# Kernel tuning notes

Hardware: AMD Instinct MI355X
Metric: run time of the kernel (lower is better)

The kernel has to match this reference:

```python
import jax, jax.numpy as jnp
import numpy as np
from functools import partial

# Static configuration (must match setup_inputs / init_kwargs)
N_CLOUDS = 16      # number of point clouds in the batch
PTS = 16384        # points per cloud (uniform, batch vector is repeat(arange(B), PTS))
RATIO = 0.25       # EncodeLayer ratio
M = int(PTS * RATIO)  # samples per cloud = 4096


def _fps_one(p, m):
    """Farthest point sampling on one cloud p:[n,3] -> local indices [m].
    Matches torch_geometric fps with random_start=False semantics: start at point 0,
    then iteratively pick the point with max min-distance to the selected set."""
    d0 = jnp.sum((p - p[0]) ** 2, axis=-1)  # squared dist to first pick, [n]

    def step(dists, _):
        idx = jnp.argmax(dists)
        new_d = jnp.sum((p - p[idx]) ** 2, axis=-1)
        return jnp.minimum(dists, new_d), idx

    _, idxs = jax.lax.scan(step, d0, None, length=m - 1)
    return jnp.concatenate([jnp.zeros((1,), dtype=idxs.dtype), idxs])


def setup_inputs() -> dict:
    key = jax.random.key(0)
    k1, k2 = jax.random.split(key)
    pos = jax.random.normal(k1, (N_CLOUDS * PTS, 3), dtype=jnp.float32)
    feats = jax.random.normal(k2, (N_CLOUDS * PTS, 128), dtype=jnp.float32)
    batch = jnp.repeat(jnp.arange(N_CLOUDS, dtype=jnp.int64), PTS)
    return {"pos": pos, "feats": feats, "batch": batch}


def reference(pos, feats, batch):
    # pos:[N,3]; batch assumed uniform with N_CLOUDS clouds of PTS points each.
    pos_b = pos.reshape(N_CLOUDS, PTS, 3)
    local = jax.vmap(partial(_fps_one, m=M))(pos_b)  # [B, M] local indices
    offsets = (jnp.arange(N_CLOUDS, dtype=local.dtype) * PTS)[:, None]
    samples = (local + offsets).reshape(-1)  # global flat indices, like torch_geometric fps
    return samples
```

## Files before the change

### kernel.cpp

```cpp
#include <hip/hip_runtime.h>

#define N_CLOUDS 16
#define PTS      16384
#define M        4096
#define FPS_THREADS  1024
#define NWAVES   (FPS_THREADS / 64)
#define PPT      16
#define SORT_THREADS 512

typedef float v2f __attribute__((ext_vector_type(2)));
typedef unsigned long long u64;
typedef unsigned int u32;
typedef unsigned short u16;


#define PAIRS8_X(X) X(0) X(1) X(2) X(3) X(4) X(5) X(6) X(7)

#define DPP_MAX_STEP(key, CTRL) { \
        const u32 lo_  = (u32)(key); \
        const u32 hi_  = (u32)((key) >> 32); \
        const u32 lo2_ = (u32)__builtin_amdgcn_update_dpp(0, (int)lo_, (CTRL), 0xf, 0xf, false); \
        const u32 hi2_ = (u32)__builtin_amdgcn_update_dpp(0, (int)hi_, (CTRL), 0xf, 0xf, false); \
        const u64 ok_  = ((u64)hi2_ << 32) | lo2_; \
        (key) = (ok_ > (key)) ? ok_ : (key); \
    }

#define DPP_FMIN_STEP(v, CTRL) { \
        const int t_ = __builtin_amdgcn_update_dpp(__float_as_int(v), __float_as_int(v), (CTRL), 0xf, 0xf, false); \
        (v) = fminf((v), __int_as_float(t_)); \
    }
#define DPP_FMAX_STEP(v, CTRL) { \
        const int t_ = __builtin_amdgcn_update_dpp(__float_as_int(v), __float_as_int(v), (CTRL), 0xf, 0xf, false); \
        (v) = fmaxf((v), __int_as_float(t_)); \
    }
#define DPP_RED6(MACRO, v) \
        MACRO(v, 0x111) MACRO(v, 0x112) MACRO(v, 0x114) MACRO(v, 0x118) \
        MACRO(v, 0x142) MACRO(v, 0x143)

__global__ __launch_bounds__(SORT_THREADS)
void sort_kernel(const float* __restrict__ pos, float* __restrict__ pos_s,
                 u16* __restrict__ mapT)
{
    __shared__ u32 keys[PTS];
    const int cloud = blockIdx.x;
    const int tid   = threadIdx.x;
    const int ln    = tid & 63;
    const size_t b3 = (size_t)cloud * PTS * 3;

    float mn = 1e30f, mx = -1e30f;
    for (int s = 0; s < PTS / SORT_THREADS; ++s) {
        const float x = pos[b3 + (size_t)(tid + s * SORT_THREADS) * 3];
        mn = fminf(mn, x);
        mx = fmaxf(mx, x);
    }
    DPP_RED6(DPP_FMIN_STEP, mn)
    DPP_RED6(DPP_FMAX_STEP, mx)
    float* red = (float*)keys;
    const int nw = SORT_THREADS / 64;
    if (ln == 63) { red[tid >> 6] = mn; red[nw + (tid >> 6)] = mx; }
    __syncthreads();
    float xmin = red[0], xmax = red[nw];
    for (int w = 1; w < nw; ++w) {
        xmin = fminf(xmin, red[w]);
        xmax = fmaxf(xmax, red[nw + w]);
    }
    __syncthreads();

    const float scale = 262143.0f / fmaxf(xmax - xmin, 1e-30f);
    for (int s = 0; s < PTS / SORT_THREADS; ++s) {
        const int i = tid + s * SORT_THREADS;
        const float x = pos[b3 + (size_t)i * 3];
        const u32 q = (u32)fminf(fmaxf((x - xmin) * scale, 0.0f), 262143.0f);
        keys[i] = (q << 14) | (u32)i;
    }

    for (u32 k = 2; k <= (u32)PTS; k <<= 1) {
        for (u32 j = k >> 1; j; j >>= 1) {
            __syncthreads();
            for (int s = 0; s < PTS / SORT_THREADS; ++s) {
                const u32 i = (u32)(tid + s * SORT_THREADS);
                const u32 p = i ^ j;
                if (p > i) {
                    const u32 a = keys[i], b = keys[p];
                    if (((i & k) == 0) == (a > b)) { keys[i] = b; keys[p] = a; }
                }
            }
        }
    }
    __syncthreads();

    for (int c = 0; c < 2; ++c) {
        u32 loc[PPT];
        const int cb = tid * 32 + c * PPT;
        for (int s = 0; s < PPT; ++s) loc[s] = keys[cb + s] & (u32)(PTS - 1);
        for (int a = 1; a < PPT; ++a) {
            const u32 v = loc[a];
            int b = a;
            while (b > 0 && loc[b - 1] > v) { loc[b] = loc[b - 1]; --b; }
            loc[b] = v;
        }
        for (int s = 0; s < PPT; ++s) keys[cb + s] = loc[s];
    }
    __syncthreads();

    for (int s = 0; s < PTS / SORT_THREADS; ++s) {
        const int i = tid + s * SORT_THREADS;
        const u32 orig = keys[i];
        mapT[(size_t)cloud * PTS + (size_t)(i & (PPT - 1)) * FPS_THREADS + (i >> 4)] = (u16)orig;
        const size_t so = b3 + (size_t)i * 3;
        const size_t oo = b3 + (size_t)orig * 3;
        pos_s[so + 0] = pos[oo + 0];
        pos_s[so + 1] = pos[oo + 1];
        pos_s[so + 2] = pos[oo + 2];
    }
}

template<bool SORTED>
__global__ __launch_bounds__(FPS_THREADS)
__attribute__((amdgpu_waves_per_eu(4, 4)))
void fps_kernel(const float* __restrict__ pos,
                const float* __restrict__ psrc,
                const u16* __restrict__ mapT,
                int* __restrict__ out)
{
#pragma clang fp contract(off)
    const int cloud = blockIdx.x;
    const int tid   = threadIdx.x;
    const int base  = cloud * PTS;
    const int wave  = tid >> 6;
    const int lane  = tid & 63;

    __shared__ u64 skey[2][NWAVES];
    __shared__ __attribute__((aligned(16))) u16 mlds[PTS];

    if constexpr (SORTED) {
        const uint4* src = (const uint4*)(mapT + (size_t)cloud * PTS);
        uint4* dst = (uint4*)mlds;
#pragma unroll
        for (int s = 0; s < PTS * 2 / 16 / FPS_THREADS; ++s)
            dst[s * FPS_THREADS + tid] = src[s * FPS_THREADS + tid];
        __syncthreads();
    }

    const float q0x = pos[(size_t)base * 3 + 0];
    const float q0y = pos[(size_t)base * 3 + 1];
    const float q0z = pos[(size_t)base * 3 + 2];
    v2f qx2 = {q0x, q0x}, qy2 = {q0y, q0y}, qz2 = {q0z, q0z};

    const float4* pos4 = (const float4*)psrc;
    const int fo = cloud * (PTS * 3 / 4) + tid * (PPT * 3 / 4);

#define DECL(j) v2f XX##j, YY##j, ZZ##j, DD##j;
    PAIRS8_X(DECL)
#undef DECL

#define QUADLOAD(q, j0, j1) { \
        const float4 fa = pos4[fo + 3*(q) + 0]; \
        const float4 fb = pos4[fo + 3*(q) + 1]; \
        const float4 fc = pos4[fo + 3*(q) + 2]; \
        XX##j0 = (v2f){fa.x, fa.w}; \
        YY##j0 = (v2f){fa.y, fb.x}; \
        ZZ##j0 = (v2f){fa.z, fb.y}; \
        XX##j1 = (v2f){fb.z, fc.y}; \
        YY##j1 = (v2f){fb.w, fc.z}; \
        ZZ##j1 = (v2f){fc.x, fc.w}; }
    QUADLOAD(0, 0, 1) QUADLOAD(1, 2, 3) QUADLOAD(2, 4, 5) QUADLOAD(3, 6, 7)
#undef QUADLOAD

#define PIN8(a,b,c,d,e,g,h,k) asm volatile("" : "+v"(a),"+v"(b),"+v"(c),"+v"(d),"+v"(e),"+v"(g),"+v"(h),"+v"(k));
    PIN8(XX0, XX1, XX2, XX3, XX4, XX5, XX6, XX7)
    PIN8(YY0, YY1, YY2, YY3, YY4, YY5, YY6, YY7)
    PIN8(ZZ0, ZZ1, ZZ2, ZZ3, ZZ4, ZZ5, ZZ6, ZZ7)
#undef PIN8

    float wxlo, wxhi;
    {
        float mn = fminf(XX0.x, XX0.y);
        float mx = fmaxf(XX0.x, XX0.y);
#define MINMAX(j) { mn = fminf(mn, fminf(XX##j.x, XX##j.y)); \
                    mx = fmaxf(mx, fmaxf(XX##j.x, XX##j.y)); }
        MINMAX(1) MINMAX(2) MINMAX(3) MINMAX(4) MINMAX(5) MINMAX(6) MINMAX(7)
#undef MINMAX
        DPP_RED6(DPP_FMIN_STEP, mn)
        DPP_RED6(DPP_FMAX_STEP, mx)
        wxlo = __int_as_float(__builtin_amdgcn_readlane(__float_as_int(mn), 63));
        wxhi = __int_as_float(__builtin_amdgcn_readlane(__float_as_int(mx), 63));
    }

    float bd = -1.0f;
    int   bk = 0;
#define INITP(j) { \
        v2f dx = XX##j - qx2; \
        v2f dy = YY##j - qy2; \
        v2f dz = ZZ##j - qz2; \
        v2f nd = (dx * dx + dy * dy) + dz * dz; \
        DD##j = nd; \
        if (nd.x > bd) { bd = nd.x; bk = 2*(j); } \
        if (nd.y > bd) { bd = nd.y; bk = 2*(j) + 1; } \
    }
    PAIRS8_X(INITP)
#undef INITP

    if (tid == 0) out[cloud * M] = base;

    u32 c_hi, c_lo;
    {
        int bi;
        if constexpr (SORTED) bi = (int)mlds[(bk << 10) + tid];
        else                  bi = tid * PPT + bk;
        u64 key = ((u64)__float_as_uint(bd) << 32) | (u32)(~bi);
        DPP_MAX_STEP(key, 0x111)
        DPP_MAX_STEP(key, 0x112)
        DPP_MAX_STEP(key, 0x114)
        DPP_MAX_STEP(key, 0x118)
        DPP_MAX_STEP(key, 0x142)
        DPP_MAX_STEP(key, 0x143)
        c_hi = (u32)__builtin_amdgcn_readlane((int)(u32)(key >> 32), 63);
        c_lo = (u32)__builtin_amdgcn_readlane((int)(u32)key, 63);
    }

    for (int i = 1; i < M; ++i) {
        if (lane == 0) skey[i & 1][wave] = ((u64)c_hi << 32) | c_lo;
        __syncthreads();

        u64 key2 = skey[i & 1][lane & 15];
        DPP_MAX_STEP(key2, 0x111)
        DPP_MAX_STEP(key2, 0x112)
        DPP_MAX_STEP(key2, 0x114)
        DPP_MAX_STEP(key2, 0x118)
        const u32 wlo = (u32)__builtin_amdgcn_readlane((int)(u32)key2, 15);
        const int wi  = (int)(~wlo);

        if (tid == 0) out[cloud * M + i] = base + wi;

        const float* qp = pos + (size_t)(base + wi) * 3;
        const float qx = qp[0], qy = qp[1], qz = qp[2];

        const float dlo  = wxlo - qx;
        const float dhi  = qx - wxhi;
        const float dgap = fmaxf(fmaxf(dlo, dhi), 0.0f);
        const float lb   = (dgap * dgap) * 0.9999f;
        if (!(lb > __uint_as_float(c_hi))) {
            qx2 = (v2f){qx, qx}; qy2 = (v2f){qy, qy}; qz2 = (v2f){qz, qz};
            bd = -1.0f; bk = 0;
#define UPD(j) { \
        v2f dx = XX##j - qx2; \
        v2f dy = YY##j - qy2; \
        v2f dz = ZZ##j - qz2; \
        v2f nd = (dx * dx + dy * dy) + dz * dz; \
        DD##j.x = fminf(DD##j.x, nd.x); \
        DD##j.y = fminf(DD##j.y, nd.y); \
        if (DD##j.x > bd) { bd = DD##j.x; bk = 2*(j); } \
        if (DD##j.y > bd) { bd = DD##j.y; bk = 2*(j) + 1; } \
    }
            PAIRS8_X(UPD)
#undef UPD
            int bi;
            if constexpr (SORTED) bi = (int)mlds[(bk << 10) + tid];
            else                  bi = tid * PPT + bk;
            u64 key = ((u64)__float_as_uint(bd) << 32) | (u32)(~bi);
            DPP_MAX_STEP(key, 0x111)
            DPP_MAX_STEP(key, 0x112)
            DPP_MAX_STEP(key, 0x114)
            DPP_MAX_STEP(key, 0x118)
            DPP_MAX_STEP(key, 0x142)
            DPP_MAX_STEP(key, 0x143)
            c_hi = (u32)__builtin_amdgcn_readlane((int)(u32)(key >> 32), 63);
            c_lo = (u32)__builtin_amdgcn_readlane((int)(u32)key, 63);
        }
    }
}

extern "C" void kernel_launch(void* const* d_in, const int* in_sizes, int n_in,
                              void* d_out, int out_size, void* d_ws, size_t ws_size,
                              hipStream_t stream) {
    const float* pos = (const float*)d_in[0];
    int* out = (int*)d_out;

    const size_t pos_s_bytes = (size_t)N_CLOUDS * PTS * 3 * sizeof(float);
    const size_t map_bytes   = (size_t)N_CLOUDS * PTS * sizeof(u16);
    if (d_ws && ws_size >= pos_s_bytes + map_bytes) {
        float* pos_s = (float*)d_ws;
        u16*   mapT  = (u16*)((char*)d_ws + pos_s_bytes);
        sort_kernel<<<N_CLOUDS, SORT_THREADS, 0, stream>>>(pos, pos_s, mapT);
        fps_kernel<true><<<N_CLOUDS, FPS_THREADS, 0, stream>>>(pos, pos_s, mapT, out);
    } else {
        fps_kernel<false><<<N_CLOUDS, FPS_THREADS, 0, stream>>>(pos, pos, nullptr, out);
    }
}
```

Measured before the change: 4.051 ms.

## Partition points into x-slabs then y-sorted tiles for tighter FPS culling bounds

The preprocessing sort now sorts points by x and then re-sorts each 4096-point chunk by y, so each wave's points form a compact x-y tile instead of a thin x-slab. In the FPS loop each wave checks a 2D bounding-box lower bound (x and y gap) against its current max distance and skips the distance update when the new sample cannot reduce any of its distances. The goal is to skip more per-wave updates per iteration, at the cost of a second bitonic sort pass in the pre-kernel and a few more scalar ops per iteration.

```diff
diff --git a/kernel.cpp b/kernel.cpp
--- a/kernel.cpp
+++ b/kernel.cpp
@@ -47,34 +47,69 @@
     const int ln    = tid & 63;
     const size_t b3 = (size_t)cloud * PTS * 3;
 
-    float mn = 1e30f, mx = -1e30f;
+    float mnx = 1e30f, mxx = -1e30f, mny = 1e30f, mxy = -1e30f;
     for (int s = 0; s < PTS / SORT_THREADS; ++s) {
-        const float x = pos[b3 + (size_t)(tid + s * SORT_THREADS) * 3];
-        mn = fminf(mn, x);
-        mx = fmaxf(mx, x);
-    }
-    DPP_RED6(DPP_FMIN_STEP, mn)
-    DPP_RED6(DPP_FMAX_STEP, mx)
+        const size_t o = b3 + (size_t)(tid + s * SORT_THREADS) * 3;
+        const float x = pos[o + 0];
+        const float y = pos[o + 1];
+        mnx = fminf(mnx, x); mxx = fmaxf(mxx, x);
+        mny = fminf(mny, y); mxy = fmaxf(mxy, y);
+    }
+    DPP_RED6(DPP_FMIN_STEP, mnx)
+    DPP_RED6(DPP_FMAX_STEP, mxx)
+    DPP_RED6(DPP_FMIN_STEP, mny)
+    DPP_RED6(DPP_FMAX_STEP, mxy)
     float* red = (float*)keys;
     const int nw = SORT_THREADS / 64;
-    if (ln == 63) { red[tid >> 6] = mn; red[nw + (tid >> 6)] = mx; }
-    __syncthreads();
-    float xmin = red[0], xmax = red[nw];
+    if (ln == 63) {
+        red[tid >> 6]          = mnx;
+        red[nw + (tid >> 6)]   = mxx;
+        red[2*nw + (tid >> 6)] = mny;
+        red[3*nw + (tid >> 6)] = mxy;
+    }
+    __syncthreads();
+    float xmin = red[0], xmax = red[nw], ymin = red[2*nw], ymax = red[3*nw];
     for (int w = 1; w < nw; ++w) {
         xmin = fminf(xmin, red[w]);
         xmax = fmaxf(xmax, red[nw + w]);
-    }
-    __syncthreads();
-
-    const float scale = 262143.0f / fmaxf(xmax - xmin, 1e-30f);
+        ymin = fminf(ymin, red[2*nw + w]);
+        ymax = fmaxf(ymax, red[3*nw + w]);
+    }
+    __syncthreads();
+
+    const float xscale = 262143.0f / fmaxf(xmax - xmin, 1e-30f);
+    const float yscale = 262143.0f / fmaxf(ymax - ymin, 1e-30f);
     for (int s = 0; s < PTS / SORT_THREADS; ++s) {
         const int i = tid + s * SORT_THREADS;
         const float x = pos[b3 + (size_t)i * 3];
-        const u32 q = (u32)fminf(fmaxf((x - xmin) * scale, 0.0f), 262143.0f);
+        const u32 q = (u32)fminf(fmaxf((x - xmin) * xscale, 0.0f), 262143.0f);
         keys[i] = (q << 14) | (u32)i;
     }
 
     for (u32 k = 2; k <= (u32)PTS; k <<= 1) {
+        for (u32 j = k >> 1; j; j >>= 1) {
+            __syncthreads();
+            for (int s = 0; s < PTS / SORT_THREADS; ++s) {
+                const u32 i = (u32)(tid + s * SORT_THREADS);
+                const u32 p = i ^ j;
+                if (p > i) {
+                    const u32 a = keys[i], b = keys[p];
+                    if (((i & k) == 0) == (a > b)) { keys[i] = b; keys[p] = a; }
+                }
+            }
+        }
+    }
+    __syncthreads();
+
+    for (int s = 0; s < PTS / SORT_THREADS; ++s) {
+        const int i = tid + s * SORT_THREADS;
+        const u32 orig = keys[i] & (u32)(PTS - 1);
+        const float y = pos[b3 + (size_t)orig * 3 + 1];
+        const u32 q = (u32)fminf(fmaxf((y - ymin) * yscale, 0.0f), 262143.0f);
+        keys[i] = (q << 14) | orig;
+    }
+
+    for (u32 k = 2; k <= 4096u; k <<= 1) {
         for (u32 j = k >> 1; j; j >>= 1) {
             __syncthreads();
             for (int s = 0; s < PTS / SORT_THREADS; ++s) {
@@ -173,18 +208,24 @@
     PIN8(ZZ0, ZZ1, ZZ2, ZZ3, ZZ4, ZZ5, ZZ6, ZZ7)
 #undef PIN8
 
-    float wxlo, wxhi;
+    float wxlo, wxhi, wylo, wyhi;
     {
-        float mn = fminf(XX0.x, XX0.y);
-        float mx = fmaxf(XX0.x, XX0.y);
-#define MINMAX(j) { mn = fminf(mn, fminf(XX##j.x, XX##j.y)); \
-                    mx = fmaxf(mx, fmaxf(XX##j.x, XX##j.y)); }
+        float mnx = fminf(XX0.x, XX0.y), mxx = fmaxf(XX0.x, XX0.y);
+        float mny = fminf(YY0.x, YY0.y), mxy = fmaxf(YY0.x, YY0.y);
+#define MINMAX(j) { mnx = fminf(mnx, fminf(XX##j.x, XX##j.y)); \
+                    mxx = fmaxf(mxx, fmaxf(XX##j.x, XX##j.y)); \
+                    mny = fminf(mny, fminf(YY##j.x, YY##j.y)); \
+                    mxy = fmaxf(mxy, fmaxf(YY##j.x, YY##j.y)); }
         MINMAX(1) MINMAX(2) MINMAX(3) MINMAX(4) MINMAX(5) MINMAX(6) MINMAX(7)
 #undef MINMAX
-        DPP_RED6(DPP_FMIN_STEP, mn)
-        DPP_RED6(DPP_FMAX_STEP, mx)
-        wxlo = __int_as_float(__builtin_amdgcn_readlane(__float_as_int(mn), 63));
-        wxhi = __int_as_float(__builtin_amdgcn_readlane(__float_as_int(mx), 63));
+        DPP_RED6(DPP_FMIN_STEP, mnx)
+        DPP_RED6(DPP_FMAX_STEP, mxx)
+        DPP_RED6(DPP_FMIN_STEP, mny)
+        DPP_RED6(DPP_FMAX_STEP, mxy)
+        wxlo = __int_as_float(__builtin_amdgcn_readlane(__float_as_int(mnx), 63));
+        wxhi = __int_as_float(__builtin_amdgcn_readlane(__float_as_int(mxx), 63));
+        wylo = __int_as_float(__builtin_amdgcn_readlane(__float_as_int(mny), 63));
+        wyhi = __int_as_float(__builtin_amdgcn_readlane(__float_as_int(mxy), 63));
     }
 
     float bd = -1.0f;
@@ -236,10 +277,9 @@
         const float* qp = pos + (size_t)(base + wi) * 3;
         const float qx = qp[0], qy = qp[1], qz = qp[2];
 
-        const float dlo  = wxlo - qx;
-        const float dhi  = qx - wxhi;
-        const float dgap = fmaxf(fmaxf(dlo, dhi), 0.0f);
-        const float lb   = (dgap * dgap) * 0.9999f;
+        const float dxg = fmaxf(fmaxf(wxlo - qx, qx - wxhi), 0.0f);
+        const float dyg = fmaxf(fmaxf(wylo - qy, qy - wyhi), 0.0f);
+        const float lb  = (dxg * dxg + dyg * dyg) * 0.9999f;
         if (!(lb > __uint_as_float(c_hi))) {
             qx2 = (v2f){qx, qx}; qy2 = (v2f){qy, qy}; qz2 = (v2f){qz, qz};
             bd = -1.0f; bk = 0;
```

After: 4.186 ms. 1.03x slower.
